# Optimization experiments

Hardware: AMD Instinct MI355X
Metric: run time of the kernel (lower is better)

Reference implementation:

```python
import jax, jax.numpy as jnp
import numpy as np

EPSILON = 0.01        # temperature
DIST_THRESH = 0.2
NUM_ITERS = 8         # sparse_rebalance_iters (== num_iters here)
TOPK = 64             # topk_support
NEG_INF = -1e9


def setup_inputs() -> dict:
    key = jax.random.key(0)
    k1, k2, k3 = jax.random.split(key, 3)
    B, N, M, D = 4, 4096, 4096, 128
    return {
        "source_feats": jax.random.normal(k1, (B, N, D), dtype=jnp.float32),
        "source_locs": jax.random.uniform(k2, (B, N, 2), dtype=jnp.float32),
        "target_locs": jax.random.uniform(k3, (B, M, 2), dtype=jnp.float32),
        "source_valid_mask": jnp.ones((B, N), dtype=bool),
        "target_valid_mask": jnp.ones((B, M), dtype=bool),
    }


def _sinkhorn_attn(source_locs, target_locs, source_valid_mask, target_valid_mask):
    # pairwise squared distances: [B, M, N]
    diff = target_locs[:, :, None, :] - source_locs[:, None, :, :]
    dist_sq = jnp.sum(diff * diff, axis=-1)
    log_k = -dist_sq / (EPSILON + 1e-8)
    valid = (dist_sq < DIST_THRESH ** 2)
    valid = valid & source_valid_mask[:, None, :] & target_valid_mask[:, :, None]

    B, M, N = valid.shape
    topk = min(TOPK, N)
    if topk < N:
        masked_log_k = jnp.where(valid, log_k, NEG_INF)
        _, topk_idx = jax.lax.top_k(masked_log_k, topk)  # [B, M, topk]
        support = jnp.zeros_like(valid).at[
            jnp.arange(B)[:, None, None], jnp.arange(M)[None, :, None], topk_idx
        ].set(True)
        valid = valid & support

    log_k = jnp.where(valid, log_k, NEG_INF)

    v = jnp.zeros((B, 1, N), dtype=log_k.dtype)
    u = jnp.zeros((B, M, 1), dtype=log_k.dtype)
    for _ in range(NUM_ITERS):
        u = -jax.nn.logsumexp(log_k + v, axis=2, keepdims=True)
        v = -jax.nn.logsumexp(log_k + u, axis=1, keepdims=True)
        v = jnp.where(source_valid_mask[:, None, :], v, 0.0)

    attn = jnp.exp(log_k + u + v)              # [B, M, N]
    has_source = valid.any(axis=-1, keepdims=True)  # [B, M, 1]
    return attn, has_source


def reference(source_feats, source_locs, target_locs, source_valid_mask, target_valid_mask):
    attn, has_source = _sinkhorn_attn(source_locs, target_locs,
                                      source_valid_mask, target_valid_mask)
    target_feats = jnp.einsum('bmn,bnd->bmd', attn, source_feats)
    target_feats = target_feats * target_valid_mask[:, :, None].astype(target_feats.dtype)
    target_feats = target_feats * has_source.astype(target_feats.dtype)
    return target_feats
```

## Files before the change

kernel.cpp:

```cpp
#include <hip/hip_runtime.h>
#include <math.h>

#define B 4
#define N 4096
#define M 4096
#define D 128
#define K 64
#define BT 256
#define WPB 4
#define RPW 4
#define CAP 768
#define CUTCAP 128
#define PC 128
#define SCAP 1536
#define EPS_DENOM 0.01000001f
#define THRESH2 0.04f
#define GC 16

__device__ __forceinline__ unsigned bf16hi(float f){
    unsigned u = __float_as_uint(f);
    return (u + 0x7FFFu + ((u >> 16) & 1u)) & 0xFFFF0000u;
}

__global__ __launch_bounds__(1024) void k_sort(const float* __restrict__ slocs,
        const float* __restrict__ tlocs,
        float4* __restrict__ sPack, float4* __restrict__ tPack,
        int* __restrict__ cellStart,
        int* __restrict__ colcnt, int* __restrict__ E, int* __restrict__ R,
        float* __restrict__ extraF, float* __restrict__ ics){
    __shared__ int hist[256], startS[256], fill[256], wtot[4];
    __shared__ float2 loc[N];
    __shared__ unsigned short scell[N];
    const int blk = blockIdx.x, tid = threadIdx.x;
    const bool tgt = blk >= B;
    const int b = tgt ? (blk - B) : blk;
    const int lane = tid & 63, w = tid >> 6;
    const float2* slp = (const float2*)((tgt ? tlocs : slocs) + (size_t)b * N * 2);
    float4* outPack = (tgt ? tPack : sPack) + (size_t)b * N;

    if (!tgt){
        for (int i = tid; i < N; i += 1024){
            colcnt[b * N + i] = 0;
            ics[b * N + i] = 1.0f;
        }
        if (b == 0){
            if (tid < B){ E[tid] = 0; R[tid] = 0; }
            if (tid < B * D) extraF[tid] = 0.f;
        }
    }

    if (tid < 256){ hist[tid] = 0; fill[tid] = 0; }
    __syncthreads();
    for (int i = tid; i < N; i += 1024){
        float2 p = slp[i];
        int cx = min(GC - 1, max(0, (int)(p.x * (float)GC)));
        int cy = min(GC - 1, max(0, (int)(p.y * (float)GC)));
        int cell = cy * GC + cx;
        loc[i] = p; scell[i] = (unsigned short)cell;
        atomicAdd(&hist[cell], 1);
    }
    __syncthreads();
    int hv = (tid < 256) ? hist[tid] : 0;
    int pre = hv;
    #pragma unroll
    for (int o = 1; o < 64; o <<= 1){ int t2 = __shfl_up(pre, o, 64); if (lane >= o) pre += t2; }
    if (tid < 256 && lane == 63) wtot[w] = pre;
    __syncthreads();
    if (tid < 256){
        int off = 0;
        for (int i = 0; i < w; ++i) off += wtot[i];
        int st = off + pre - hv;
        startS[tid] = st;
        if (!tgt) cellStart[b * 257 + tid] = st;
    }
    if (!tgt && tid == 0) cellStart[b * 257 + 256] = N;
    __syncthreads();
    for (int i = tid; i < N; i += 1024){
        int cell = scell[i];
        int pos = startS[cell] + atomicAdd(&fill[cell], 1);
        float2 p = loc[i];
        outPack[pos] = make_float4(p.x, p.y, __int_as_float(i), 0.f);
    }
}

__global__ __launch_bounds__(BT, 5) void k_build(const float4* __restrict__ sPack,
        const int* __restrict__ cellStart, const float4* __restrict__ tPack,
        unsigned* __restrict__ csrP, int* __restrict__ cnt,
        int* __restrict__ colcnt, unsigned* __restrict__ cscP,
        int* __restrict__ R, float* __restrict__ rs){
    __shared__ int cs[257];
    __shared__ float2 sxy[SCAP];
    __shared__ int    sid[SCAP];
    __shared__ unsigned short cj[WPB][CAP];
    __shared__ int   hist[WPB][64];
    __shared__ float cutd[WPB][CUTCAP];
    __shared__ int   cutn[WPB][CUTCAP];
    __shared__ float4 rowT[16];
    __shared__ int gB[16], gL[16], lB[16];
    __shared__ int stot;

    const int bid  = blockIdx.x;
    const int sb   = (bid & 7) * 128 + (bid >> 3);
    const int b    = sb >> 8;
    const int s00  = (sb & 255) * (WPB * RPW);
    const int tid  = threadIdx.x;
    const int w    = tid >> 6;
    const int lane = tid & 63;
    const unsigned long long pmask = (lane == 0) ? 0ull : ((1ull << lane) - 1);
    const float4* sp = sPack + (size_t)b * N;
    const float4* tp = tPack + (size_t)b * M;

    for (int i = tid; i < 257; i += BT) cs[i] = cellStart[b * 257 + i];
    if (tid < 16) rowT[tid] = tp[s00 + tid];
    __syncthreads();

    float txmin = 1e9f, txmax = -1e9f, tymin = 1e9f, tymax = -1e9f;
    #pragma unroll
    for (int i = 0; i < 16; ++i){
        float4 t = rowT[i];
        txmin = fminf(txmin, t.x); txmax = fmaxf(txmax, t.x);
        tymin = fminf(tymin, t.y); tymax = fmaxf(tymax, t.y);
    }
    const int bcy0 = max(0, (int)floorf((tymin - 0.2f) * (float)GC - 0.001f));
    const int bcy1 = min(GC - 1, (int)floorf((tymax + 0.2f) * (float)GC + 0.001f));
    const int ncy  = bcy1 - bcy0 + 1;
    if (tid < ncy && tid < 16){
        int cy = bcy0 + tid;
        float rowLo = cy * 0.0625f, rowHi = rowLo + 0.0625f;
        float dymin = fmaxf(0.f, fmaxf(rowLo - tymax, tymin - rowHi));
        float dxm = sqrtf(fmaxf(THRESH2 - dymin * dymin + 1e-5f, 0.f));
        int cx0 = max(0, (int)floorf((txmin - dxm) * (float)GC - 0.001f));
        int cx1 = min(GC - 1, (int)floorf((txmax + dxm) * (float)GC + 0.001f));
        int s = cs[cy * GC + cx0], e = cs[cy * GC + cx1 + 1];
        gB[tid] = s; gL[tid] = e - s;
    }
    __syncthreads();
    if (tid == 0){
        if (ncy > 16) stot = SCAP + 1;
        else {
            int acc = 0;
            for (int i = 0; i < ncy; ++i){ lB[i] = acc; acc += gL[i]; }
            stot = acc;
        }
    }
    __syncthreads();
    const bool staged = (stot <= SCAP);
    if (staged){
        for (int i = 0; i < ncy; ++i){
            int s = gB[i], len = gL[i], l0 = lB[i];
            for (int j = tid; j < len; j += BT){
                float4 q = sp[s + j];
                sxy[l0 + j] = make_float2(q.x, q.y);
                sid[l0 + j] = ((s + j) << 16) | __float_as_int(q.z);
            }
        }
    }
    __syncthreads();

    for (int r = 0; r < RPW; ++r){
        const int srt   = s00 + w * RPW + r;
        const int srid  = b * M + srt;
        const float4 t  = rowT[w * RPW + r];
        const float tx  = t.x;
        const float ty  = t.y;

        hist[w][lane] = 0;
        float rsum = 0.f;

        const int cy0 = max(0, (int)floorf((ty - 0.2f) * (float)GC - 0.001f));
        const int cy1 = min(GC - 1, (int)floorf((ty + 0.2f) * (float)GC + 0.001f));

        int c = 0;
        for (int cy = cy0; cy <= cy1; ++cy){
            float rowLo = cy * 0.0625f, rowHi = rowLo + 0.0625f;
            float dymin = fmaxf(0.f, fmaxf(rowLo - ty, ty - rowHi));
            float dxm = sqrtf(fmaxf(THRESH2 - dymin * dymin + 1e-5f, 0.f));
            int cx0 = max(0, (int)floorf((tx - dxm) * (float)GC - 0.001f));
            int cx1 = min(GC - 1, (int)floorf((tx + dxm) * (float)GC + 0.001f));
            int s = cs[cy * GC + cx0], e = cs[cy * GC + cx1 + 1];
            int len = e - s;
            int base_l = staged ? (lB[cy - bcy0] + (s - gB[cy - bcy0])) : s;
            for (int j0 = 0; j0 < len; j0 += 64){
                int i = j0 + lane;
                bool valid = i < len;
                int lp = base_l + i;
                float d2 = 1e9f;
                if (valid){
                    float qx, qy;
                    if (staged){ float2 q = sxy[lp]; qx = q.x; qy = q.y; }
                    else       { float4 q = sp[lp];  qx = q.x; qy = q.y; }
                    float dx = __fsub_rn(tx, qx);
                    float dy = __fsub_rn(ty, qy);
                    d2 = __fadd_rn(__fmul_rn(dx, dx), __fmul_rn(dy, dy));
                }
                bool in = valid && (d2 < THRESH2);
                unsigned long long ml = __ballot(in);
                if (in){
                    int p = c + __popcll(ml & pmask);
                    if (p < CAP) cj[w][p] = (unsigned short)lp;
                    atomicAdd(&hist[w][min((int)(d2 * 1600.0f), 63)], 1);
                }
                c += __popcll(ml);
            }
        }
        const int ctot = min(c, CAP);

        int h = hist[w][lane];
        int pre = h;
        #pragma unroll
        for (int o = 1; o < 64; o <<= 1){
            int t2 = __shfl_up(pre, o, 64);
            if (lane >= o) pre += t2;
        }
        int cutB = 64, q = 0;
        if (c > K){
            unsigned long long ge = __ballot(pre >= K);
            int fb = __ffsll((long long)ge) - 1;
            cutB = fb;
            q = K - __shfl(pre - h, fb, 64);
        }

        int base = 0, cutc = 0;
        for (int i0 = 0; i0 < ctot; i0 += 64){
            int i = i0 + lane;
            bool valid = i < ctot;
            float d2 = 1e9f; int pk = 0;
            if (valid){
                int lp = cj[w][i];
                float qx, qy;
                if (staged){ float2 q = sxy[lp]; qx = q.x; qy = q.y; pk = sid[lp]; }
                else       { float4 q = sp[lp];  qx = q.x; qy = q.y;
                             pk = (lp << 16) | __float_as_int(q.z); }
                float dx = __fsub_rn(tx, qx);
                float dy = __fsub_rn(ty, qy);
                d2 = __fadd_rn(__fmul_rn(dx, dx), __fmul_rn(dy, dy));
            }
            int bk = valid ? min((int)(d2 * 1600.0f), 63) : 64;
            bool low = valid && (bk < cutB);
            unsigned long long ml = __ballot(low);
            if (low){
                int p = base + __popcll(ml & pmask);
                unsigned eb = bf16hi(expf(-(d2 / EPS_DENOM)));
                rsum += __uint_as_float(eb);
                int cpos = pk >> 16;
                csrP[(size_t)srid * K + p] = eb | (unsigned)cpos;
                int bn = (b << 12) + cpos;
                int slot = atomicAdd(&colcnt[bn], 1);
                if (slot < PC)
                    cscP[(size_t)bn * PC + slot] = eb | (unsigned)srt;
            }
            base += __popcll(ml);
            if (cutB < 64){
                bool eq = valid && (bk == cutB);
                unsigned long long me = __ballot(eq);
                if (eq){
                    int p = cutc + __popcll(me & pmask);
                    if (p < CUTCAP){ cutd[w][p] = d2; cutn[w][p] = pk; }
                }
                cutc += __popcll(me);
            }
        }

        if (c > K){
            int cc = min(cutc, CUTCAP);
            for (int i0 = 0; i0 < CUTCAP; i0 += 64){
                int i = i0 + lane;
                bool sel = false; float d2i = 0.f; int ni = 0;
                if (i < cc){
                    d2i = cutd[w][i]; ni = cutn[w][i];
                    int rank = 0;
                    for (int j = 0; j < cc; ++j){
                        float dj = cutd[w][j]; int nj = cutn[w][j];
                        rank += (dj < d2i) || (dj == d2i && (nj & 0xFFFF) < (ni & 0xFFFF));
                    }
                    sel = rank < q;
                }
                unsigned long long ms = __ballot(sel);
                if (sel){
                    int p = base + __popcll(ms & pmask);
                    unsigned eb = bf16hi(expf(-(d2i / EPS_DENOM)));
                    rsum += __uint_as_float(eb);
                    int cpos = ni >> 16;
                    csrP[(size_t)srid * K + p] = eb | (unsigned)cpos;
                    int bn = (b << 12) + cpos;
                    int slot = atomicAdd(&colcnt[bn], 1);
                    if (slot < PC)
                        cscP[(size_t)bn * PC + slot] = eb | (unsigned)srt;
                }
                base += __popcll(ms);
                if (i0 + 64 >= cc) break;
            }
            if (lane == 0) cnt[srid] = K;
        } else {
            if (lane == 0){
                cnt[srid] = c;
                if (c == 0) atomicAdd(&R[b], 1);
            }
        }
        #pragma unroll
        for (int o = 32; o; o >>= 1) rsum += __shfl_xor(rsum, o, 64);
        if (lane == 0) rs[srid] = rsum;
    }
}

__global__ __launch_bounds__(256) void k_prep(const int* __restrict__ colcnt,
        int* __restrict__ E, const float* __restrict__ feats,
        const float4* __restrict__ sPack, float* __restrict__ extraF){
    int t = blockIdx.x * blockDim.x + threadIdx.x;
    int lane = t & 63, b = t >> 12;
    int cc = colcnt[t];
    unsigned long long em = __ballot(cc == 0);
    if (lane == 0 && em) atomicAdd(&E[b], __popcll(em));
    if (cc == 0){
        int orig = __float_as_int(sPack[t].z);
        for (int d = 0; d < D; ++d)
            atomicAdd(&extraF[b * D + d], feats[((size_t)((b << 12) + orig)) * D + d]);
    }
}

__global__ __launch_bounds__(256) void kA(const unsigned* __restrict__ csrP,
        const int* __restrict__ cnt,
        const float* __restrict__ ics, const int* __restrict__ E,
        float* __restrict__ eu){
    int t = blockIdx.x * blockDim.x + threadIdx.x;
    int rid = t >> 6, lane = t & 63;
    int b = rid >> 12;
    int c = cnt[rid];
    float s = 0.f;
    if (lane < c){
        unsigned pe = csrP[(size_t)rid * K + lane];
        s = __uint_as_float(pe & 0xFFFF0000u) * ics[(b << 12) + (pe & 0xFFFFu)];
    }
    #pragma unroll
    for (int o = 32; o; o >>= 1) s += __shfl_xor(s, o, 64);
    int Eb = E[b];
    if (c == 0 && Eb == 0){
        if (lane == 0) eu[rid] = 0.f;
    } else {
        if (Eb > 0) s += (float)Eb;
        if (lane == 0) eu[rid] = 1.0f / s;
    }
}

__global__ __launch_bounds__(256) void kB(const unsigned* __restrict__ cscP,
        const int* __restrict__ colcnt,
        const float* __restrict__ eu, const int* __restrict__ R,
        float* __restrict__ ics,
        const float* __restrict__ rs, const int* __restrict__ E, int first){
    int t = blockIdx.x * blockDim.x + threadIdx.x;
    int cid = t >> 6, lane = t & 63;
    int b = cid >> 12;
    int cc = min(colcnt[cid], PC);
    float s = 0.f;
    if (first){
        float Eb = (float)E[b];
        for (int p = lane; p < cc; p += 64){
            unsigned pe = cscP[(size_t)cid * PC + p];
            float euv = 1.0f / (rs[(b << 12) + (pe & 0xFFFFu)] + Eb);
            s += __uint_as_float(pe & 0xFFFF0000u) * euv;
        }
    } else {
        for (int p = lane; p < cc; p += 64){
            unsigned pe = cscP[(size_t)cid * PC + p];
            s += __uint_as_float(pe & 0xFFFF0000u) * eu[(b << 12) + (pe & 0xFFFFu)];
        }
    }
    #pragma unroll
    for (int o = 32; o; o >>= 1) s += __shfl_xor(s, o, 64);
    if (lane == 0)
        ics[cid] = 1.0f / (s + (float)R[b]);
}

__global__ __launch_bounds__(128) void k_out(const float* __restrict__ feats,
        const unsigned* __restrict__ csrP,
        const int* __restrict__ cnt, const float* __restrict__ eu,
        const float* __restrict__ ics, const float* __restrict__ extraF,
        const float4* __restrict__ sPack, const float4* __restrict__ tPack,
        float* __restrict__ out){
    __shared__ float att[K];
    __shared__ int   sidx[K];
    int bid = blockIdx.x;
    int sg  = (bid & 7) * 2048 + (bid >> 3);
    int b   = sg >> 12;
    int srt = sg & 4095;
    int m   = __float_as_int(tPack[(size_t)b * M + srt].z);
    const float4* sp = sPack + (size_t)b * N;
    int tid = threadIdx.x;
    int c = cnt[sg];
    if (tid < K){
        float a = 0.f; int ix = 0;
        if (tid < c){
            unsigned pe = csrP[(size_t)sg * K + tid];
            int cpos = pe & 0xFFFFu;
            a = __uint_as_float(pe & 0xFFFF0000u) * eu[sg] * ics[(b << 12) + cpos];
            ix = __float_as_int(sp[cpos].z);
        }
        att[tid] = a; sidx[tid] = ix;
    }
    __syncthreads();
    float acc = 0.f;
    if (c > 0){
        acc = extraF[b * D + tid];
        for (int k = 0; k < c; ++k)
            acc += att[k] * feats[((size_t)((b << 12) + sidx[k])) * D + tid];
    }
    out[((size_t)((b << 12) + m)) * D + tid] = acc;
}

extern "C" void kernel_launch(void* const* d_in, const int* in_sizes, int n_in,
                              void* d_out, int out_size, void* d_ws, size_t ws_size,
                              hipStream_t stream){
    const float* feats = (const float*)d_in[0];
    const float* slocs = (const float*)d_in[1];
    const float* tlocs = (const float*)d_in[2];
    float* out = (float*)d_out;

    char* w = (char*)d_ws;
    size_t off = 0;
    auto carve = [&](size_t bytes) -> void* {
        void* p = w + off;
        off += (bytes + 255) & ~(size_t)255;
        return p;
    };
    unsigned* csrP  = (unsigned*)carve((size_t)B * M * K * 4);
    unsigned* cscP  = (unsigned*)carve((size_t)B * N * PC * 4);
    int*   cnt     = (int*)  carve((size_t)B * M * 4);
    int*   colcnt  = (int*)  carve((size_t)B * N * 4);
    float* eu      = (float*)carve((size_t)B * M * 4);
    float* ics     = (float*)carve((size_t)B * N * 4);
    float* rs      = (float*)carve((size_t)B * M * 4);
    int*   E       = (int*)  carve(B * 4);
    int*   R       = (int*)  carve(B * 4);
    float* extraF  = (float*)carve((size_t)B * D * 4);
    float4* sPack  = (float4*)carve((size_t)B * N * 16);
    float4* tPack  = (float4*)carve((size_t)B * M * 16);
    int*   cellStart = (int*)carve((size_t)B * 257 * 4);

    k_sort<<<2 * B, 1024, 0, stream>>>(slocs, tlocs, sPack, tPack, cellStart,
                                       colcnt, E, R, extraF, ics);
    k_build<<<B * M / (WPB * RPW), BT, 0, stream>>>(sPack, cellStart, tPack,
            csrP, cnt, colcnt, cscP, R, rs);
    k_prep<<<(B * N) / 256, 256, 0, stream>>>(colcnt, E, feats, sPack, extraF);

    kB<<<B * N / 4, 256, 0, stream>>>(cscP, colcnt, eu, R, ics, rs, E, 1);
    for (int it = 1; it < 8; ++it){
        kA<<<B * M / 4, 256, 0, stream>>>(csrP, cnt, ics, E, eu);
        kB<<<B * N / 4, 256, 0, stream>>>(cscP, colcnt, eu, R, ics, rs, E, 0);
    }
    k_out<<<B * M, D, 0, stream>>>(feats, csrP, cnt, eu, ics, extraF, sPack, tPack, out);
}
```

Before: 232.2 us.

## Fuse row and column Sinkhorn passes via atomic scatter into row accumulators

Removes the separate row-normalisation kernel kA. The column kernel now scatters each entry's weight times the new column scale into a per-iteration row accumulator with atomics. The next iteration, and the output kernel, read that accumulator directly to form the row scale. This halves the kernel launches in the Sinkhorn loop and drops the CSR gather pass. In exchange it adds float atomics, with nondeterministic summation order, plus zero-init of seven accumulator buffers in k_sort. The new column kernel also assumes at most 128 entries per column (two fixed loads), which matches the existing PC cap.

```diff
diff --git a/kernel.cpp b/kernel.cpp
--- a/kernel.cpp
+++ b/kernel.cpp
@@ -16,6 +16,7 @@
 #define EPS_DENOM 0.01000001f
 #define THRESH2 0.04f
 #define GC 16
+#define BM (B * M)
 
 __device__ __forceinline__ unsigned bf16hi(float f){
     unsigned u = __float_as_uint(f);
@@ -27,7 +28,7 @@
         float4* __restrict__ sPack, float4* __restrict__ tPack,
         int* __restrict__ cellStart,
         int* __restrict__ colcnt, int* __restrict__ E, int* __restrict__ R,
-        float* __restrict__ extraF, float* __restrict__ ics){
+        float* __restrict__ extraF, float* __restrict__ racc){
     __shared__ int hist[256], startS[256], fill[256], wtot[4];
     __shared__ float2 loc[N];
     __shared__ unsigned short scell[N];
@@ -39,10 +40,10 @@
     float4* outPack = (tgt ? tPack : sPack) + (size_t)b * N;
 
     if (!tgt){
-        for (int i = tid; i < N; i += 1024){
-            colcnt[b * N + i] = 0;
-            ics[b * N + i] = 1.0f;
-        }
+        for (int i = tid; i < N; i += 1024) colcnt[b * N + i] = 0;
+        for (int it2 = 1; it2 < 8; ++it2)
+            for (int i = tid; i < M; i += 1024)
+                racc[it2 * BM + b * M + i] = 0.f;
         if (b == 0){
             if (tid < B){ E[tid] = 0; R[tid] = 0; }
             if (tid < B * D) extraF[tid] = 0.f;
@@ -87,7 +88,7 @@
         const int* __restrict__ cellStart, const float4* __restrict__ tPack,
         unsigned* __restrict__ csrP, int* __restrict__ cnt,
         int* __restrict__ colcnt, unsigned* __restrict__ cscP,
-        int* __restrict__ R, float* __restrict__ rs){
+        int* __restrict__ R, float* __restrict__ racc0){
     __shared__ int cs[257];
     __shared__ float2 sxy[SCAP];
     __shared__ int    sid[SCAP];
@@ -299,7 +300,7 @@
         }
         #pragma unroll
         for (int o = 32; o; o >>= 1) rsum += __shfl_xor(rsum, o, 64);
-        if (lane == 0) rs[srid] = rsum;
+        if (lane == 0) racc0[srid] = rsum;
     }
 }
 
@@ -318,65 +319,47 @@
     }
 }
 
-__global__ __launch_bounds__(256) void kA(const unsigned* __restrict__ csrP,
-        const int* __restrict__ cnt,
-        const float* __restrict__ ics, const int* __restrict__ E,
-        float* __restrict__ eu){
-    int t = blockIdx.x * blockDim.x + threadIdx.x;
-    int rid = t >> 6, lane = t & 63;
-    int b = rid >> 12;
-    int c = cnt[rid];
-    float s = 0.f;
-    if (lane < c){
-        unsigned pe = csrP[(size_t)rid * K + lane];
-        s = __uint_as_float(pe & 0xFFFF0000u) * ics[(b << 12) + (pe & 0xFFFFu)];
-    }
-    #pragma unroll
-    for (int o = 32; o; o >>= 1) s += __shfl_xor(s, o, 64);
-    int Eb = E[b];
-    if (c == 0 && Eb == 0){
-        if (lane == 0) eu[rid] = 0.f;
-    } else {
-        if (Eb > 0) s += (float)Eb;
-        if (lane == 0) eu[rid] = 1.0f / s;
-    }
-}
-
 __global__ __launch_bounds__(256) void kB(const unsigned* __restrict__ cscP,
         const int* __restrict__ colcnt,
-        const float* __restrict__ eu, const int* __restrict__ R,
-        float* __restrict__ ics,
-        const float* __restrict__ rs, const int* __restrict__ E, int first){
+        const float* __restrict__ prevAcc, float* __restrict__ nextAcc,
+        const int* __restrict__ R, float* __restrict__ ics,
+        const int* __restrict__ E, int doScatter){
     int t = blockIdx.x * blockDim.x + threadIdx.x;
     int cid = t >> 6, lane = t & 63;
     int b = cid >> 12;
     int cc = min(colcnt[cid], PC);
+    float Eb = (float)E[b];
+    const float* pa = prevAcc + (b << 12);
     float s = 0.f;
-    if (first){
-        float Eb = (float)E[b];
-        for (int p = lane; p < cc; p += 64){
-            unsigned pe = cscP[(size_t)cid * PC + p];
-            float euv = 1.0f / (rs[(b << 12) + (pe & 0xFFFFu)] + Eb);
-            s += __uint_as_float(pe & 0xFFFF0000u) * euv;
-        }
-    } else {
-        for (int p = lane; p < cc; p += 64){
-            unsigned pe = cscP[(size_t)cid * PC + p];
-            s += __uint_as_float(pe & 0xFFFF0000u) * eu[(b << 12) + (pe & 0xFFFFu)];
-        }
+    unsigned pe0 = 0, pe1 = 0;
+    bool h0 = lane < cc, h1 = lane + 64 < cc;
+    if (h0){
+        pe0 = cscP[(size_t)cid * PC + lane];
+        s = __uint_as_float(pe0 & 0xFFFF0000u) / (pa[pe0 & 0xFFFFu] + Eb);
+    }
+    if (h1){
+        pe1 = cscP[(size_t)cid * PC + lane + 64];
+        s += __uint_as_float(pe1 & 0xFFFF0000u) / (pa[pe1 & 0xFFFFu] + Eb);
     }
     #pragma unroll
     for (int o = 32; o; o >>= 1) s += __shfl_xor(s, o, 64);
-    if (lane == 0)
-        ics[cid] = 1.0f / (s + (float)R[b]);
+    float icsv = 1.0f / (s + (float)R[b]);
+    if (lane == 0) ics[cid] = icsv;
+    if (doScatter){
+        float* na = nextAcc + (b << 12);
+        if (h0) atomicAdd(&na[pe0 & 0xFFFFu],
+                          __uint_as_float(pe0 & 0xFFFF0000u) * icsv);
+        if (h1) atomicAdd(&na[pe1 & 0xFFFFu],
+                          __uint_as_float(pe1 & 0xFFFF0000u) * icsv);
+    }
 }
 
 __global__ __launch_bounds__(128) void k_out(const float* __restrict__ feats,
         const unsigned* __restrict__ csrP,
-        const int* __restrict__ cnt, const float* __restrict__ eu,
+        const int* __restrict__ cnt, const float* __restrict__ racc7,
         const float* __restrict__ ics, const float* __restrict__ extraF,
         const float4* __restrict__ sPack, const float4* __restrict__ tPack,
-        float* __restrict__ out){
+        const int* __restrict__ E, float* __restrict__ out){
     __shared__ float att[K];
     __shared__ int   sidx[K];
     int bid = blockIdx.x;
@@ -390,9 +373,10 @@
     if (tid < K){
         float a = 0.f; int ix = 0;
         if (tid < c){
+            float euv = 1.0f / (racc7[sg] + (float)E[b]);
             unsigned pe = csrP[(size_t)sg * K + tid];
             int cpos = pe & 0xFFFFu;
-            a = __uint_as_float(pe & 0xFFFF0000u) * eu[sg] * ics[(b << 12) + cpos];
+            a = __uint_as_float(pe & 0xFFFF0000u) * euv * ics[(b << 12) + cpos];
             ix = __float_as_int(sp[cpos].z);
         }
         att[tid] = a; sidx[tid] = ix;
@@ -426,9 +410,8 @@
     unsigned* cscP  = (unsigned*)carve((size_t)B * N * PC * 4);
     int*   cnt     = (int*)  carve((size_t)B * M * 4);
     int*   colcnt  = (int*)  carve((size_t)B * N * 4);
-    float* eu      = (float*)carve((size_t)B * M * 4);
     float* ics     = (float*)carve((size_t)B * N * 4);
-    float* rs      = (float*)carve((size_t)B * M * 4);
+    float* racc    = (float*)carve((size_t)8 * BM * 4);
     int*   E       = (int*)  carve(B * 4);
     int*   R       = (int*)  carve(B * 4);
     float* extraF  = (float*)carve((size_t)B * D * 4);
@@ -437,15 +420,16 @@
     int*   cellStart = (int*)carve((size_t)B * 257 * 4);
 
     k_sort<<<2 * B, 1024, 0, stream>>>(slocs, tlocs, sPack, tPack, cellStart,
-                                       colcnt, E, R, extraF, ics);
+                                       colcnt, E, R, extraF, racc);
     k_build<<<B * M / (WPB * RPW), BT, 0, stream>>>(sPack, cellStart, tPack,
-            csrP, cnt, colcnt, cscP, R, rs);
+            csrP, cnt, colcnt, cscP, R, racc );
     k_prep<<<(B * N) / 256, 256, 0, stream>>>(colcnt, E, feats, sPack, extraF);
 
-    kB<<<B * N / 4, 256, 0, stream>>>(cscP, colcnt, eu, R, ics, rs, E, 1);
-    for (int it = 1; it < 8; ++it){
-        kA<<<B * M / 4, 256, 0, stream>>>(csrP, cnt, ics, E, eu);
-        kB<<<B * N / 4, 256, 0, stream>>>(cscP, colcnt, eu, R, ics, rs, E, 0);
-    }
-    k_out<<<B * M, D, 0, stream>>>(feats, csrP, cnt, eu, ics, extraF, sPack, tPack, out);
-}
+    for (int it = 1; it <= 8; ++it){
+        kB<<<B * N / 4, 256, 0, stream>>>(cscP, colcnt,
+                racc + (size_t)(it - 1) * BM, racc + (size_t)(it & 7) * BM,
+                R, ics, E, it < 8 ? 1 : 0);
+    }
+    k_out<<<B * M, D, 0, stream>>>(feats, csrP, cnt, racc + (size_t)7 * BM,
+            ics, extraF, sPack, tPack, E, out);
+}
```

Measured after the change: 283.3 us. 1.22x slower.
